# Kernel optimization log

Hardware: AMD Instinct MI355X
Metric: run time of the kernel (lower is better)

Reference implementation:

```python
import jax, jax.numpy as jnp
import numpy as np

B, H, L, D = 8, 8, 2048, 64
FACTOR = 5


def _num_sel(length):
    return min(int(FACTOR * np.ceil(np.log(length))), length)


def setup_inputs() -> dict:
    key = jax.random.key(0)
    kq, kk, kv, ki = jax.random.split(key, 4)
    num_k = _num_sel(L)
    return {
        "q": jax.random.normal(kq, (B, H, L, D), dtype=jnp.float32),
        "k": jax.random.normal(kk, (B, H, L, D), dtype=jnp.float32),
        "v": jax.random.normal(kv, (B, H, L, D), dtype=jnp.float32),
        "random_index": jax.random.randint(ki, (L, num_k), 0, L, dtype=jnp.int32),
    }


def reference(q, k, v, random_index):
    b, h, q_len, d = q.shape
    k_len = k.shape[2]
    num_q = _num_sel(q_len)

    # --- random K sampling per query: k_s[b,h,i,j,:] = k[b,h,random_index[i,j],:]
    k_s = k[:, :, random_index, :]                      # (B,H,L,num_k,D)
    pre_attn = jnp.einsum('bhid,bhijd->bhij', q, k_s)   # (B,H,L,num_k)
    measure = pre_attn.max(-1) - pre_attn.sum(-1) / k_len  # (B,H,L)

    # --- top-k query selection (sorted=False in torch; order-insensitive math)
    _, idx = jax.lax.top_k(measure, num_q)              # (B,H,num_q)
    q_sel = jnp.take_along_axis(q, idx[..., None], axis=2)  # (B,H,num_q,D)

    # --- reduced attention over all keys
    attn = jnp.einsum('bhid,bhjd->bhij', q_sel, k) * (d ** -0.5)  # (B,H,num_q,k_len)

    # ProbMask: causal mask per selected query index (mask where j > idx[i])
    mask = jnp.arange(k_len)[None, None, None, :] > idx[..., None]
    attn = jnp.where(mask, -jnp.inf, attn)
    attn = jax.nn.softmax(attn, axis=-1)

    out_sel = jnp.einsum('bhij,bhjd->bhid', attn, v)    # (B,H,num_q,D)

    # --- context initialization (use_mask=True branch) and scatter back
    context = jnp.cumsum(v, axis=2)                     # (B,H,L,D)
    bi = jnp.arange(b)[:, None, None]
    hi = jnp.arange(h)[None, :, None]
    out = context.at[bi, hi, idx].set(out_sel)          # (B,H,L,D)
    return out, attn
```

## Files before the change

kernel.cpp:

```cpp
#include <hip/hip_runtime.h>
#include <float.h>
#include <math.h>

#define B_  8
#define H_  8
#define L_  2048
#define D_  64
#define NS  40
#define BH  (B_*H_)
#define SCALE 0.125f

__global__ __launch_bounds__(256) void measure_kernel(
    const float* __restrict__ q, const float* __restrict__ k,
    const int* __restrict__ ridx, float* __restrict__ measure)
{
    int wave = threadIdx.x >> 6, lane = threadIdx.x & 63;
    int qid = blockIdx.x * 4 + wave;
    int bh  = qid >> 11;
    int i   = qid & (L_ - 1);
    int qj  = lane >> 4;
    int d4  = lane & 15;

    int rs = ridx[i * NS + (lane < NS ? lane : NS - 1)];

    const float4* kb = (const float4*)(k + (size_t)bh * L_ * D_);
    float4 qq = ((const float4*)(q + ((size_t)bh * L_ + i) * D_))[d4];

    float mx = -FLT_MAX, sm = 0.f;
    #pragma unroll
    for (int p = 0; p < 10; ++p) {
        int j = p * 4 + qj;
        int r = __shfl(rs, j, 64);
        float4 kk = kb[(size_t)r * 16 + d4];
        float pp = qq.x*kk.x + qq.y*kk.y + qq.z*kk.z + qq.w*kk.w;
        pp += __shfl_xor(pp, 1, 64);
        pp += __shfl_xor(pp, 2, 64);
        pp += __shfl_xor(pp, 4, 64);
        pp += __shfl_xor(pp, 8, 64);
        mx = fmaxf(mx, pp);
        sm += pp;
    }
    mx = fmaxf(mx, __shfl_xor(mx, 16, 64));  sm += __shfl_xor(sm, 16, 64);
    mx = fmaxf(mx, __shfl_xor(mx, 32, 64));  sm += __shfl_xor(sm, 32, 64);
    if (lane == 0)
        measure[(size_t)bh * L_ + i] = mx - sm * (1.0f / (float)L_);
}

__global__ __launch_bounds__(256) void topk_kernel(
    const float* __restrict__ measure, int* __restrict__ idxOut)
{
    __shared__ float wv[4]; __shared__ int wi[4];
    __shared__ float bvS;   __shared__ int biS;
    int bh = blockIdx.x, t = threadIdx.x;
    const float4* m4 = (const float4*)(measure + (size_t)bh * L_);
    float vals[8];
    float4 a = m4[t*2], b = m4[t*2 + 1];
    vals[0]=a.x; vals[1]=a.y; vals[2]=a.z; vals[3]=a.w;
    vals[4]=b.x; vals[5]=b.y; vals[6]=b.z; vals[7]=b.w;

    float lv = -FLT_MAX; int li = t*8;
    #pragma unroll
    for (int e = 0; e < 8; ++e) if (vals[e] > lv) { lv = vals[e]; li = t*8 + e; }

    int lane = t & 63, w = t >> 6;
    for (int r = 0; r < NS; ++r) {
        float v = lv; int idx = li;
        #pragma unroll
        for (int off = 32; off; off >>= 1) {
            float ov = __shfl_xor(v, off, 64);
            int   oi = __shfl_xor(idx, off, 64);
            if (ov > v || (ov == v && oi < idx)) { v = ov; idx = oi; }
        }
        if (lane == 0) { wv[w] = v; wi[w] = idx; }
        __syncthreads();
        if (t == 0) {
            float bv = wv[0]; int bi = wi[0];
            #pragma unroll
            for (int ww = 1; ww < 4; ++ww)
                if (wv[ww] > bv || (wv[ww] == bv && wi[ww] < bi)) { bv = wv[ww]; bi = wi[ww]; }
            bvS = bv; biS = bi;
            idxOut[bh * NS + r] = bi;
        }
        __syncthreads();
        int bi = biS;
        if ((bi >> 3) == t) {
            #pragma unroll
            for (int e = 0; e < 8; ++e) if ((bi & 7) == e) vals[e] = -FLT_MAX;
            lv = -FLT_MAX; li = t*8;
            #pragma unroll
            for (int e = 0; e < 8; ++e) if (vals[e] > lv) { lv = vals[e]; li = t*8 + e; }
        }
        __syncthreads();
    }
}

__global__ __launch_bounds__(256) void cumsum_p1(
    const float* __restrict__ v, float4* __restrict__ vpart)
{
    __shared__ float4 part[16][16];
    int bh = blockIdx.x >> 4, c = blockIdx.x & 15;
    int d4 = threadIdx.x & 15, sub = threadIdx.x >> 4;
    const float4* vb = (const float4*)(v + (size_t)bh * L_ * D_);
    int r0 = c*128 + sub*8;
    float4 s = make_float4(0,0,0,0);
    #pragma unroll
    for (int r = 0; r < 8; ++r) {
        float4 x = vb[(r0 + r)*16 + d4];
        s.x += x.x; s.y += x.y; s.z += x.z; s.w += x.w;
    }
    part[sub][d4] = s;
    __syncthreads();
    if (sub == 0) {
        float4 tot = part[0][d4];
        #pragma unroll
        for (int ss = 1; ss < 16; ++ss) {
            float4 x = part[ss][d4];
            tot.x += x.x; tot.y += x.y; tot.z += x.z; tot.w += x.w;
        }
        vpart[(bh*16 + c)*16 + d4] = tot;
    }
}

__global__ __launch_bounds__(256) void cumsum_p2(
    const float* __restrict__ v, const float4* __restrict__ vpart,
    float* __restrict__ out)
{
    __shared__ float4 part[16][16];
    int bh = blockIdx.x >> 4, c = blockIdx.x & 15;
    int d4 = threadIdx.x & 15, sub = threadIdx.x >> 4;
    const float4* vb = (const float4*)(v + (size_t)bh * L_ * D_);
    float4*       ob = (float4*)(out + (size_t)bh * L_ * D_);
    int r0 = c*128 + sub*8;
    float4 s = make_float4(0,0,0,0);
    #pragma unroll
    for (int r = 0; r < 8; ++r) {
        float4 x = vb[(r0 + r)*16 + d4];
        s.x += x.x; s.y += x.y; s.z += x.z; s.w += x.w;
    }
    part[sub][d4] = s;
    float4 run = make_float4(0,0,0,0);
    for (int cc = 0; cc < c; ++cc) {
        float4 x = vpart[(bh*16 + cc)*16 + d4];
        run.x += x.x; run.y += x.y; run.z += x.z; run.w += x.w;
    }
    __syncthreads();
    #pragma unroll
    for (int ss = 0; ss < 16; ++ss) {
        if (ss < sub) {
            float4 x = part[ss][d4];
            run.x += x.x; run.y += x.y; run.z += x.z; run.w += x.w;
        }
    }
    #pragma unroll
    for (int r = 0; r < 8; ++r) {
        float4 x = vb[(r0 + r)*16 + d4];
        run.x += x.x; run.y += x.y; run.z += x.z; run.w += x.w;
        ob[(r0 + r)*16 + d4] = run;
    }
}

__global__ __launch_bounds__(256) void scores_kernel(
    const float* __restrict__ q, const float* __restrict__ k,
    const int* __restrict__ idxSel, float* __restrict__ attn)
{
    __shared__ float4 kbuf[16 * 129];
    int bh = blockIdx.x / 10, grp = blockIdx.x % 10;
    int qi = threadIdx.x >> 6, sub = threadIdx.x & 63;
    int rank = grp*4 + qi;
    int qrow = idxSel[bh*NS + rank];

    const float4* qrp = (const float4*)(q + ((size_t)bh * L_ + qrow) * D_);
    float4 qreg[16];
    #pragma unroll
    for (int g = 0; g < 16; ++g) qreg[g] = qrp[g];

    const float4* kb = (const float4*)(k + (size_t)bh * L_ * D_);
    float sc0[16], sc1[16];

    #pragma unroll
    for (int c = 0; c < 16; ++c) {
        __syncthreads();
        int j0 = c * 128;
        #pragma unroll
        for (int it = 0; it < 8; ++it) {
            int fi = threadIdx.x + 256*it;
            int g = fi & 15, j = fi >> 4;
            kbuf[g*129 + j] = kb[(size_t)(j0 + j)*16 + g];
        }
        __syncthreads();
        float acc0 = 0.f, acc1 = 0.f;
        #pragma unroll
        for (int g = 0; g < 16; ++g) {
            float4 k0 = kbuf[g*129 + sub];
            float4 k1 = kbuf[g*129 + sub + 64];
            float4 qq = qreg[g];
            acc0 += qq.x*k0.x + qq.y*k0.y + qq.z*k0.z + qq.w*k0.w;
            acc1 += qq.x*k1.x + qq.y*k1.y + qq.z*k1.z + qq.w*k1.w;
        }
        sc0[c] = acc0 * SCALE;
        sc1[c] = acc1 * SCALE;
    }

    float mx = -FLT_MAX;
    #pragma unroll
    for (int c = 0; c < 16; ++c) {
        if (c*128 + sub      <= qrow) mx = fmaxf(mx, sc0[c]);
        if (c*128 + sub + 64 <= qrow) mx = fmaxf(mx, sc1[c]);
    }
    #pragma unroll
    for (int off = 32; off; off >>= 1) mx = fmaxf(mx, __shfl_xor(mx, off, 64));

    float sum = 0.f;
    #pragma unroll
    for (int c = 0; c < 16; ++c) {
        sc0[c] = (c*128 + sub      <= qrow) ? __expf(sc0[c] - mx) : 0.f;
        sc1[c] = (c*128 + sub + 64 <= qrow) ? __expf(sc1[c] - mx) : 0.f;
        sum += sc0[c] + sc1[c];
    }
    #pragma unroll
    for (int off = 32; off; off >>= 1) sum += __shfl_xor(sum, off, 64);
    float inv = 1.f / sum;

    float* arow = attn + (size_t)(bh*NS + rank) * L_;
    #pragma unroll
    for (int c = 0; c < 16; ++c) {
        arow[c*128 + sub]      = sc0[c] * inv;
        arow[c*128 + sub + 64] = sc1[c] * inv;
    }
}

__global__ __launch_bounds__(256) void pv_kernel(
    const float* __restrict__ v, const int* __restrict__ idxSel,
    const float* __restrict__ attn, float* __restrict__ out)
{
    __shared__ float wl[L_ + 64];
    __shared__ float4 part[16][16];
    int bh = blockIdx.x / NS, r = blockIdx.x % NS;
    int qrow = idxSel[bh*NS + r];
    const float4* ar = (const float4*)(attn + (size_t)(bh*NS + r) * L_);
    int t = threadIdx.x;

    #pragma unroll
    for (int it = 0; it < 2; ++it) {
        int f = t + 256*it;
        float4 x = ar[f];
        int j = 4*f;
        *((float4*)&wl[j + 4*(j >> 7)]) = x;
    }
    __syncthreads();

    int d4 = t & 15, seg = t >> 4;
    const float4* vb = (const float4*)(v + (size_t)bh * L_ * D_);
    float4 acc = make_float4(0,0,0,0);
    int jlo = seg*128, jhi = min(jlo + 127, qrow);
    for (int j = jlo; j <= jhi; ++j) {
        float wgt = wl[j + 4*(j >> 7)];
        float4 x = vb[(size_t)j*16 + d4];
        acc.x += wgt*x.x; acc.y += wgt*x.y; acc.z += wgt*x.z; acc.w += wgt*x.w;
    }
    part[seg][d4] = acc;
    __syncthreads();
    for (int s2 = 8; s2; s2 >>= 1) {
        if (seg < s2) {
            float4 o = part[seg + s2][d4];
            acc.x += o.x; acc.y += o.y; acc.z += o.z; acc.w += o.w;
            part[seg][d4] = acc;
        }
        __syncthreads();
    }
    if (seg == 0) {
        float4* orow = (float4*)(out + ((size_t)bh * L_ + qrow) * D_);
        orow[d4] = acc;
    }
}

extern "C" void kernel_launch(void* const* d_in, const int* in_sizes, int n_in,
                              void* d_out, int out_size, void* d_ws, size_t ws_size,
                              hipStream_t stream) {
    const float* q    = (const float*)d_in[0];
    const float* k    = (const float*)d_in[1];
    const float* v    = (const float*)d_in[2];
    const int*   ridx = (const int*)d_in[3];

    float* out     = (float*)d_out;
    float* attnOut = out + (size_t)BH * L_ * D_;

    float*  measure = (float*)d_ws;
    int*    idxSel  = (int*)((char*)d_ws + (size_t)BH * L_ * sizeof(float));
    float4* vpart   = (float4*)d_ws;

    measure_kernel<<<BH * L_ / 4, 256, 0, stream>>>(q, k, ridx, measure);
    topk_kernel   <<<BH,          256, 0, stream>>>(measure, idxSel);
    cumsum_p1     <<<BH * 16,     256, 0, stream>>>(v, vpart);
    cumsum_p2     <<<BH * 16,     256, 0, stream>>>(v, vpart, out);
    scores_kernel <<<BH * 10,     256, 0, stream>>>(q, k, idxSel, attnOut);
    pv_kernel     <<<BH * NS,     256, 0, stream>>>(v, idxSel, attnOut, out);
}
```

Baseline: 383.7 us.

## Reshape measure kernel lane mapping and batch four queries per PV block

The measure kernel now assigns four lanes per sampled key, each covering the full 64-wide dot product through four float4 loads. This removes the shuffle-based index broadcast and two of the reduction shuffle steps. The PV kernel processes four selected query rows per block, so each V row is loaded once and reused for four weight vectors, cutting global V traffic by four. In exchange, loop bounds follow the largest query index among the four (masked weights are zero), there are fewer blocks (640 instead of 2560), and more shared memory is used per block.

```diff
diff --git a/kernel.cpp b/kernel.cpp
--- a/kernel.cpp
+++ b/kernel.cpp
@@ -18,30 +18,35 @@
     int qid = blockIdx.x * 4 + wave;
     int bh  = qid >> 11;
     int i   = qid & (L_ - 1);
-    int qj  = lane >> 4;
-    int d4  = lane & 15;
-
-    int rs = ridx[i * NS + (lane < NS ? lane : NS - 1)];
+    int g   = lane >> 2;
+    int sl  = lane & 3;
 
     const float4* kb = (const float4*)(k + (size_t)bh * L_ * D_);
-    float4 qq = ((const float4*)(q + ((size_t)bh * L_ + i) * D_))[d4];
+    const float4* qp = (const float4*)(q + ((size_t)bh * L_ + i) * D_);
+
+    float4 q0 = qp[sl], q1 = qp[4 + sl], q2 = qp[8 + sl], q3 = qp[12 + sl];
 
     float mx = -FLT_MAX, sm = 0.f;
     #pragma unroll
-    for (int p = 0; p < 10; ++p) {
-        int j = p * 4 + qj;
-        int r = __shfl(rs, j, 64);
-        float4 kk = kb[(size_t)r * 16 + d4];
-        float pp = qq.x*kk.x + qq.y*kk.y + qq.z*kk.z + qq.w*kk.w;
+    for (int p = 0; p < 3; ++p) {
+        int s = p * 16 + g;
+        bool valid = (s < NS);
+        int r = ridx[i * NS + (valid ? s : NS - 1)];
+        const float4* kr = kb + (size_t)r * 16;
+        float4 k0 = kr[sl], k1 = kr[4 + sl], k2 = kr[8 + sl], k3 = kr[12 + sl];
+        float pp = q0.x*k0.x + q0.y*k0.y + q0.z*k0.z + q0.w*k0.w
+                 + q1.x*k1.x + q1.y*k1.y + q1.z*k1.z + q1.w*k1.w
+                 + q2.x*k2.x + q2.y*k2.y + q2.z*k2.z + q2.w*k2.w
+                 + q3.x*k3.x + q3.y*k3.y + q3.z*k3.z + q3.w*k3.w;
         pp += __shfl_xor(pp, 1, 64);
         pp += __shfl_xor(pp, 2, 64);
-        pp += __shfl_xor(pp, 4, 64);
-        pp += __shfl_xor(pp, 8, 64);
-        mx = fmaxf(mx, pp);
-        sm += pp;
-    }
-    mx = fmaxf(mx, __shfl_xor(mx, 16, 64));  sm += __shfl_xor(sm, 16, 64);
-    mx = fmaxf(mx, __shfl_xor(mx, 32, 64));  sm += __shfl_xor(sm, 32, 64);
+        if (valid) { mx = fmaxf(mx, pp); sm += pp; }
+    }
+    #pragma unroll
+    for (int off = 4; off < 64; off <<= 1) {
+        mx = fmaxf(mx, __shfl_xor(mx, off, 64));
+        sm += __shfl_xor(sm, off, 64);
+    }
     if (lane == 0)
         measure[(size_t)bh * L_ + i] = mx - sm * (1.0f / (float)L_);
 }
@@ -233,44 +238,61 @@
     const float* __restrict__ v, const int* __restrict__ idxSel,
     const float* __restrict__ attn, float* __restrict__ out)
 {
-    __shared__ float wl[L_ + 64];
+    __shared__ float wl[4][L_ + 64];
     __shared__ float4 part[16][16];
-    int bh = blockIdx.x / NS, r = blockIdx.x % NS;
-    int qrow = idxSel[bh*NS + r];
-    const float4* ar = (const float4*)(attn + (size_t)(bh*NS + r) * L_);
+    __shared__ int qr4[4];
+    int bh = blockIdx.x / 10, grp = blockIdx.x % 10;
     int t = threadIdx.x;
-
-    #pragma unroll
-    for (int it = 0; it < 2; ++it) {
+    if (t < 4) qr4[t] = idxSel[bh*NS + grp*4 + t];
+
+    #pragma unroll
+    for (int it = 0; it < 8; ++it) {
         int f = t + 256*it;
-        float4 x = ar[f];
-        int j = 4*f;
-        *((float4*)&wl[j + 4*(j >> 7)]) = x;
+        int rr = f >> 9, fi = f & 511;
+        const float4* ar = (const float4*)(attn + (size_t)(bh*NS + grp*4 + rr) * L_);
+        float4 x = ar[fi];
+        int j = 4*fi;
+        *((float4*)&wl[rr][j + 4*(j >> 7)]) = x;
     }
     __syncthreads();
 
+    int maxq = max(max(qr4[0], qr4[1]), max(qr4[2], qr4[3]));
     int d4 = t & 15, seg = t >> 4;
     const float4* vb = (const float4*)(v + (size_t)bh * L_ * D_);
-    float4 acc = make_float4(0,0,0,0);
-    int jlo = seg*128, jhi = min(jlo + 127, qrow);
+    float4 acc[4];
+    #pragma unroll
+    for (int rr = 0; rr < 4; ++rr) acc[rr] = make_float4(0,0,0,0);
+
+    int jlo = seg*128, jhi = min(jlo + 127, maxq);
     for (int j = jlo; j <= jhi; ++j) {
-        float wgt = wl[j + 4*(j >> 7)];
         float4 x = vb[(size_t)j*16 + d4];
-        acc.x += wgt*x.x; acc.y += wgt*x.y; acc.z += wgt*x.z; acc.w += wgt*x.w;
-    }
-    part[seg][d4] = acc;
-    __syncthreads();
-    for (int s2 = 8; s2; s2 >>= 1) {
-        if (seg < s2) {
-            float4 o = part[seg + s2][d4];
-            acc.x += o.x; acc.y += o.y; acc.z += o.z; acc.w += o.w;
-            part[seg][d4] = acc;
-        }
-        __syncthreads();
-    }
-    if (seg == 0) {
-        float4* orow = (float4*)(out + ((size_t)bh * L_ + qrow) * D_);
-        orow[d4] = acc;
+        int jp = j + 4*(j >> 7);
+        #pragma unroll
+        for (int rr = 0; rr < 4; ++rr) {
+            float wgt = wl[rr][jp];
+            acc[rr].x += wgt*x.x; acc[rr].y += wgt*x.y;
+            acc[rr].z += wgt*x.z; acc[rr].w += wgt*x.w;
+        }
+    }
+
+    #pragma unroll
+    for (int rr = 0; rr < 4; ++rr) {
+        part[seg][d4] = acc[rr];
+        __syncthreads();
+        float4 a = acc[rr];
+        for (int s2 = 8; s2; s2 >>= 1) {
+            if (seg < s2) {
+                float4 o = part[seg + s2][d4];
+                a.x += o.x; a.y += o.y; a.z += o.z; a.w += o.w;
+                part[seg][d4] = a;
+            }
+            __syncthreads();
+        }
+        if (seg == 0) {
+            float4* orow = (float4*)(out + ((size_t)bh * L_ + qr4[rr]) * D_);
+            orow[d4] = a;
+        }
+        __syncthreads();
     }
 }
 
@@ -294,5 +316,5 @@
     cumsum_p1     <<<BH * 16,     256, 0, stream>>>(v, vpart);
     cumsum_p2     <<<BH * 16,     256, 0, stream>>>(v, vpart, out);
     scores_kernel <<<BH * 10,     256, 0, stream>>>(q, k, idxSel, attnOut);
-    pv_kernel     <<<BH * NS,     256, 0, stream>>>(v, idxSel, attnOut, out);
-}
+    pv_kernel     <<<BH * 10,     256, 0, stream>>>(v, idxSel, attnOut, out);
+}
```

New measurement: 389.6 us. About the same (+1.5%).
